# Kernel optimization log

Measured on AMD Instinct MI355X. Metric: run time of the kernel, lower is better.

## Reference

```python
import jax, jax.numpy as jnp
import numpy as np

N, F, K, D = 4096, 512, 8, 64


def setup_inputs() -> dict:
    key = jax.random.key(0)
    ks = jax.random.split(key, 6)
    H = jax.random.normal(ks[0], (N, F), dtype=jnp.float32)
    # dense 0/1 adjacency with self-loops
    A = jax.random.randint(ks[1], (N, N), 0, 2).astype(jnp.float32)
    A = jnp.maximum(A, jnp.eye(N, dtype=jnp.float32))
    idx = jnp.arange(N, dtype=jnp.int64)
    glorot_w = (2.0 / (F + D)) ** 0.5
    glorot_a = (2.0 / (D + 1)) ** 0.5
    kernels = glorot_w * jax.random.normal(ks[2], (K, F, D), dtype=jnp.float32)
    attn_kernels = glorot_a * jax.random.normal(ks[3], (K, 2, D, 1), dtype=jnp.float32)
    biases = 0.01 * jax.random.normal(ks[4], (K, D), dtype=jnp.float32)
    return {"H": H, "A": A, "idx": idx, "kernels": kernels,
            "attn_kernels": attn_kernels, "biases": biases}


def reference(H, A, idx, kernels, attn_kernels, biases):
    # (dropout is identity at inference)
    batch_A = A[:, idx]                                  # [N, N]
    HW = jnp.einsum('nf,kfd->knd', H, kernels)           # [K, N, D]
    a1 = attn_kernels[:, 0, :, 0]                        # [K, D]
    a2 = attn_kernels[:, 1, :, 0]                        # [K, D]
    s1 = jnp.einsum('knd,kd->kn', HW, a1)                # score_i (source)
    s2 = jnp.einsum('knd,kd->kn', HW, a2)                # score_j (target)
    scores = s1[:, :, None] + s2[:, None, :]             # [K, N, N]
    neg_big = jnp.finfo(jnp.float32).min
    scores = jnp.where(batch_A[None, :, :] == 0.0, neg_big, scores)
    # LeakyReLU(0.2) applied AFTER masking, as in the original
    scores = jnp.where(scores >= 0, scores, 0.2 * scores)
    attn = jax.nn.softmax(scores, axis=-1)               # [K, N, N]
    res = jnp.einsum('kij,kjd->kid', attn, HW) + biases[:, None, :]  # [K, N, D]
    out = jax.nn.elu(res)                                # is_last=False -> concat heads
    out = jnp.transpose(out, (1, 0, 2)).reshape(N, K * D)
    return out
```

## Files before the change

kernel.cpp:

```cpp
#include <hip/hip_runtime.h>
#include <hip/hip_fp16.h>
#include <float.h>
#include <math.h>

#define NN 4096
#define FF 512
#define KK 8
#define DD 64

typedef float f32x4 __attribute__((ext_vector_type(4)));
typedef _Float16 h2 __attribute__((ext_vector_type(2)));
typedef _Float16 f16x4 __attribute__((ext_vector_type(4)));
typedef _Float16 f16x8 __attribute__((ext_vector_type(8)));
typedef unsigned int u32;
typedef unsigned long long u64;

__device__ __forceinline__ h2 H2(u32 u) { union { u32 u; h2 h; } x; x.u = u; return x.h; }
__device__ __forceinline__ u32 U32(h2 h) { union { u32 u; h2 h; } x; x.h = h; return x.u; }
__device__ __forceinline__ u32 pmask(u32 m, int sh) {
  u32 b = (m >> sh) & 3u;
  return ((b * 0x10001u) & 0x20001u) * 0xFFFFu;
}

__global__ __launch_bounds__(256) void k_bits(const float* __restrict__ A,
                                              u64* __restrict__ bits) {
  const int gw = (blockIdx.x * 256 + threadIdx.x) >> 6;
  const int lane = threadIdx.x & 63;
  const int nw = (gridDim.x * 256) >> 6;
  const int totw = NN * NN / 64;
  for (int wd = gw; wd < totw; wd += nw) {
    float a = A[(size_t)wd * 64 + lane];
    u64 m = __ballot(a != 0.0f);
    if (lane == 0) bits[wd] = m;
  }
}

__global__ __launch_bounds__(256) void k_hf(const float* __restrict__ H,
                                            _Float16* __restrict__ HF) {
  const int w = threadIdx.x >> 6, lane = threadIdx.x & 63;
  const int tile = blockIdx.x * 4 + w;
  const int rb = tile >> 4, fb = tile & 15;
  const int l15 = lane & 15, grp = lane >> 4;
  const float* src = H + (size_t)(rb * 16 + l15) * FF + fb * 32 + grp * 4;
  float4 lo = *reinterpret_cast<const float4*>(src);
  float4 hi = *reinterpret_cast<const float4*>(src + 16);
  f16x8 v;
  v[0] = (_Float16)lo.x; v[1] = (_Float16)lo.y; v[2] = (_Float16)lo.z; v[3] = (_Float16)lo.w;
  v[4] = (_Float16)hi.x; v[5] = (_Float16)hi.y; v[6] = (_Float16)hi.z; v[7] = (_Float16)hi.w;
  *reinterpret_cast<f16x8*>(HF + (size_t)tile * 512 + lane * 8) = v;
}

__global__ __launch_bounds__(256) void k_wf(const float* __restrict__ Wk,
                                            _Float16* __restrict__ WF) {
  const int g = blockIdx.x * 256 + threadIdx.x;
  const int frag = g >> 6, lane = g & 63;
  const int k = frag >> 6, fb = (frag >> 2) & 15, db = frag & 3;
  const int l15 = lane & 15, grp = lane >> 4;
  f16x8 v;
  #pragma unroll
  for (int e = 0; e < 8; ++e) {
    int f = fb * 32 + grp * 4 + (e & 3) + 16 * (e >> 2);
    int d = db * 16 + l15;
    v[e] = (_Float16)Wk[((size_t)k * FF + f) * DD + d];
  }
  *reinterpret_cast<f16x8*>(WF + (size_t)frag * 512 + lane * 8) = v;
}

__global__ __launch_bounds__(256) void k_hw(const _Float16* __restrict__ HF,
                                            const _Float16* __restrict__ WF,
                                            const float* __restrict__ attk,
                                            _Float16* __restrict__ HWF,
                                            float* __restrict__ s1,
                                            float* __restrict__ s2) {
  __shared__ __align__(16) _Float16 Bs[64 * 512];
  const int w = threadIdx.x >> 6, lane = threadIdx.x & 63;
  const int k = blockIdx.y;
  const int rb = blockIdx.x * 4 + w;
  const int l15 = lane & 15, grp = lane >> 4;
  const _Float16* wfk = WF + (size_t)k * 64 * 512;
  #pragma unroll
  for (int c = 0; c < 16; ++c) {
    int chunk = c * 4 + w;
    *reinterpret_cast<f16x8*>(&Bs[chunk * 512 + lane * 8]) =
        *reinterpret_cast<const f16x8*>(wfk + (size_t)chunk * 512 + lane * 8);
  }
  __syncthreads();
  f32x4 acc[4] = {};
  for (int fb = 0; fb < 16; ++fb) {
    f16x8 a = *reinterpret_cast<const f16x8*>(HF + (size_t)(rb * 16 + fb) * 512 + lane * 8);
    #pragma unroll
    for (int n = 0; n < 4; ++n) {
      f16x8 b = *reinterpret_cast<const f16x8*>(&Bs[(fb * 4 + n) * 512 + lane * 8]);
      acc[n] = __builtin_amdgcn_mfma_f32_16x16x32_f16(a, b, acc[n], 0, 0, 0);
    }
  }
  const int jb = rb >> 1;
  const int half = rb & 1;
  #pragma unroll
  for (int db = 0; db < 4; ++db) {
    f16x4 v;
    #pragma unroll
    for (int q = 0; q < 4; ++q) v[q] = (_Float16)acc[db][q];
    *reinterpret_cast<f16x4*>(HWF + (size_t)((k * 128 + jb) * 4 + db) * 512 + lane * 8 + half * 4) = v;
  }
  float a1v[4], a2v[4];
  #pragma unroll
  for (int n = 0; n < 4; ++n) {
    a1v[n] = attk[k * 2 * DD + n * 16 + l15];
    a2v[n] = attk[k * 2 * DD + DD + n * 16 + l15];
  }
  #pragma unroll
  for (int q = 0; q < 4; ++q) {
    float p1 = 0.f, p2 = 0.f;
    #pragma unroll
    for (int n = 0; n < 4; ++n) { p1 += acc[n][q] * a1v[n]; p2 += acc[n][q] * a2v[n]; }
    #pragma unroll
    for (int off = 8; off; off >>= 1) { p1 += __shfl_xor(p1, off); p2 += __shfl_xor(p2, off); }
    if (l15 == 0) {
      int row = rb * 16 + grp * 4 + q;
      s1[k * NN + row] = p1;
      s2[k * NN + row] = p2;
    }
  }
}

__global__ __launch_bounds__(256) void k_mx(const float* __restrict__ s2,
                                            float* __restrict__ mx) {
  const int k = blockIdx.x, tid = threadIdx.x;
  float m = -FLT_MAX;
  for (int j = tid; j < NN; j += 256) m = fmaxf(m, s2[k * NN + j]);
  #pragma unroll
  for (int o = 32; o; o >>= 1) m = fmaxf(m, __shfl_xor(m, o));
  __shared__ float sm[4];
  if ((tid & 63) == 0) sm[tid >> 6] = m;
  __syncthreads();
  if (tid == 0) mx[k] = fmaxf(fmaxf(sm[0], sm[1]), fmaxf(sm[2], sm[3]));
}

__global__ __launch_bounds__(256, 2) void k_attn(
    const u64* __restrict__ bits, const _Float16* __restrict__ HWF,
    const float* __restrict__ s1, const float* __restrict__ s2,
    const float* __restrict__ mx,
    _Float16* __restrict__ pacc, float* __restrict__ pw) {
  __shared__ __align__(16) _Float16 epl[1024];
  __shared__ __align__(16) _Float16 enl[1024];
  const int k = blockIdx.y, jh = blockIdx.z;
  const int i0 = blockIdx.x * 256;
  const int tid = threadIdx.x;
  const int w = tid >> 6, lane = tid & 63, l15 = lane & 15, grp = lane >> 4;
  const int jbase = jh * 1024;
  const float mxk = mx[k];
  {
    float4 sv = *reinterpret_cast<const float4*>(&s2[k * NN + jbase + tid * 4]);
    f16x4 e4, n4;
    e4[0] = (_Float16)__expf(sv.x - mxk); e4[1] = (_Float16)__expf(sv.y - mxk);
    e4[2] = (_Float16)__expf(sv.z - mxk); e4[3] = (_Float16)__expf(sv.w - mxk);
    n4[0] = (_Float16)__expf(0.2f * (sv.x - mxk)); n4[1] = (_Float16)__expf(0.2f * (sv.y - mxk));
    n4[2] = (_Float16)__expf(0.2f * (sv.z - mxk)); n4[3] = (_Float16)__expf(0.2f * (sv.w - mxk));
    *reinterpret_cast<f16x4*>(&epl[tid * 4]) = e4;
    *reinterpret_cast<f16x4*>(&enl[tid * 4]) = n4;
  }
  __syncthreads();
  h2 P1h[4], Q1h[4];
  const u64* browp[4];
  #pragma unroll
  for (int s = 0; s < 4; ++s) {
    int row = i0 + w * 64 + s * 16 + l15;
    float s1r = s1[k * NN + row];
    float t = s1r + mxk;
    float cr = fmaxf(t, 0.2f * t);
    _Float16 p = (_Float16)__expf(t - cr);
    _Float16 q = (_Float16)__expf(0.2f * t - cr);
    P1h[s] = h2{p, p}; Q1h[s] = h2{q, q};
    browp[s] = bits + (size_t)row * (NN / 64) + (jbase >> 6);
  }
  const int g4 = grp * 4;
  const _Float16* hwb = HWF + ((size_t)(k * 128 + jh * 32) * 4) * 512 + lane * 8;
  const h2 ones = h2{(_Float16)1.0f, (_Float16)1.0f};
  f32x4 acc[4][4] = {};
  float wsum[4] = {};
  u64 bw[4];
  #pragma unroll
  for (int s = 0; s < 4; ++s) bw[s] = browp[s][0];
  for (int jw = 0; jw < 16; ++jw) {
    u64 nbw[4];
    const int nx = jw < 15 ? jw + 1 : 15;
    #pragma unroll
    for (int s = 0; s < 4; ++s) nbw[s] = browp[s][nx];
    #pragma unroll
    for (int js = 0; js < 2; ++js) {
      const int jl = jw * 64 + js * 32;
      f16x8 bf0 = *reinterpret_cast<const f16x8*>(hwb + ((jw * 2 + js) * 4 + 0) * 512);
      f16x8 bf1 = *reinterpret_cast<const f16x8*>(hwb + ((jw * 2 + js) * 4 + 1) * 512);
      f16x8 bf2 = *reinterpret_cast<const f16x8*>(hwb + ((jw * 2 + js) * 4 + 2) * 512);
      f16x8 bf3 = *reinterpret_cast<const f16x8*>(hwb + ((jw * 2 + js) * 4 + 3) * 512);
      f16x4 elo = *reinterpret_cast<const f16x4*>(&epl[jl + g4]);
      f16x4 ehi = *reinterpret_cast<const f16x4*>(&epl[jl + 16 + g4]);
      f16x4 nlo = *reinterpret_cast<const f16x4*>(&enl[jl + g4]);
      f16x4 nhi = *reinterpret_cast<const f16x4*>(&enl[jl + 16 + g4]);
      const u32 e01 = ((const u32*)&elo)[0], e23 = ((const u32*)&elo)[1];
      const u32 e45 = ((const u32*)&ehi)[0], e67 = ((const u32*)&ehi)[1];
      const u32 n01 = ((const u32*)&nlo)[0], n23 = ((const u32*)&nlo)[1];
      const u32 n45 = ((const u32*)&nhi)[0], n67 = ((const u32*)&nhi)[1];
      #pragma unroll
      for (int s = 0; s < 4; ++s) {
        const u32 m32 = (u32)(bw[s] >> (js * 32));
        u32 p0 = U32(__builtin_elementwise_max(P1h[s] * H2(e01), Q1h[s] * H2(n01))) & pmask(m32, g4);
        u32 p1 = U32(__builtin_elementwise_max(P1h[s] * H2(e23), Q1h[s] * H2(n23))) & pmask(m32, g4 + 2);
        u32 p2 = U32(__builtin_elementwise_max(P1h[s] * H2(e45), Q1h[s] * H2(n45))) & pmask(m32, g4 + 16);
        u32 p3 = U32(__builtin_elementwise_max(P1h[s] * H2(e67), Q1h[s] * H2(n67))) & pmask(m32, g4 + 18);
        wsum[s] = __builtin_amdgcn_fdot2(H2(p0), ones, wsum[s], false);
        wsum[s] = __builtin_amdgcn_fdot2(H2(p1), ones, wsum[s], false);
        wsum[s] = __builtin_amdgcn_fdot2(H2(p2), ones, wsum[s], false);
        wsum[s] = __builtin_amdgcn_fdot2(H2(p3), ones, wsum[s], false);
        union { u32 u[4]; f16x8 v; } af;
        af.u[0] = p0; af.u[1] = p1; af.u[2] = p2; af.u[3] = p3;
        acc[s][0] = __builtin_amdgcn_mfma_f32_16x16x32_f16(af.v, bf0, acc[s][0], 0, 0, 0);
        acc[s][1] = __builtin_amdgcn_mfma_f32_16x16x32_f16(af.v, bf1, acc[s][1], 0, 0, 0);
        acc[s][2] = __builtin_amdgcn_mfma_f32_16x16x32_f16(af.v, bf2, acc[s][2], 0, 0, 0);
        acc[s][3] = __builtin_amdgcn_mfma_f32_16x16x32_f16(af.v, bf3, acc[s][3], 0, 0, 0);
      }
    }
    #pragma unroll
    for (int s = 0; s < 4; ++s) bw[s] = nbw[s];
  }
  const size_t ob = (size_t)(jh * KK + k) * NN;
  #pragma unroll
  for (int s = 0; s < 4; ++s) {
    float ws = wsum[s];
    ws += __shfl_xor(ws, 16);
    ws += __shfl_xor(ws, 32);
    #pragma unroll
    for (int n = 0; n < 4; ++n)
      #pragma unroll
      for (int q = 0; q < 4; ++q) {
        int row = i0 + w * 64 + s * 16 + grp * 4 + q;
        pacc[(ob + row) * DD + n * 16 + l15] = (_Float16)acc[s][n][q];
      }
    if (grp == 0) {
      int row = i0 + w * 64 + s * 16 + l15;
      pw[ob + row] = ws;
    }
  }
}

__global__ __launch_bounds__(256) void k_merge(const _Float16* __restrict__ pacc,
                                               const float* __restrict__ pw,
                                               const float* __restrict__ bias,
                                               float* __restrict__ out) {
  const int o4 = blockIdx.x * 256 + threadIdx.x;
  const int i = o4 >> 7, rem = o4 & 127, k = rem >> 4, d4 = rem & 15;
  const size_t idx = ((size_t)k * NN + i) * DD + d4 * 4;
  float4 a = {0.f, 0.f, 0.f, 0.f};
  float wsum = 0.f;
  #pragma unroll
  for (int s = 0; s < 4; ++s) {
    f16x4 v = *reinterpret_cast<const f16x4*>(&pacc[(size_t)s * (KK * NN * DD) + idx]);
    a.x += (float)v[0]; a.y += (float)v[1]; a.z += (float)v[2]; a.w += (float)v[3];
    wsum += pw[(size_t)s * (KK * NN) + k * NN + i];
  }
  float rw = 1.0f / wsum;
  float4 bv = *reinterpret_cast<const float4*>(bias + k * DD + d4 * 4);
  float4 r;
  r.x = a.x * rw + bv.x; r.x = r.x > 0.f ? r.x : expm1f(r.x);
  r.y = a.y * rw + bv.y; r.y = r.y > 0.f ? r.y : expm1f(r.y);
  r.z = a.z * rw + bv.z; r.z = r.z > 0.f ? r.z : expm1f(r.z);
  r.w = a.w * rw + bv.w; r.w = r.w > 0.f ? r.w : expm1f(r.w);
  *reinterpret_cast<float4*>(out + (size_t)o4 * 4) = r;
}

extern "C" void kernel_launch(void* const* d_in, const int* in_sizes, int n_in,
                              void* d_out, int out_size, void* d_ws, size_t ws_size,
                              hipStream_t stream) {
  const float* H    = (const float*)d_in[0];
  const float* A    = (const float*)d_in[1];
  const float* Wk   = (const float*)d_in[3];
  const float* attk = (const float*)d_in[4];
  const float* bias = (const float*)d_in[5];
  float* out = (float*)d_out;

  char* base = (char*)d_ws;
  _Float16* HF  = (_Float16*)(base + 0);
  _Float16* WF  = (_Float16*)(base + 4194304);
  _Float16* HWF = (_Float16*)(base + 4718592);
  u64* bits     = (u64*)(base + 8912896);
  float* s1p    = (float*)(base + 11010048);
  float* s2p    = (float*)(base + 11141120);
  float* mxp    = (float*)(base + 11272192);
  _Float16* pacc = (_Float16*)(base + 11276288);
  float* pwp    = (float*)(base + 28053504);

  k_bits<<<2048, 256, 0, stream>>>(A, bits);
  k_hf<<<1024, 256, 0, stream>>>(H, HF);
  k_wf<<<128, 256, 0, stream>>>(Wk, WF);
  k_hw<<<dim3(NN / 64, KK), 256, 0, stream>>>(HF, WF, attk, HWF, s1p, s2p);
  k_mx<<<KK, 256, 0, stream>>>(s2p, mxp);
  k_attn<<<dim3(NN / 256, KK, 4), 256, 0, stream>>>(bits, HWF, s1p, s2p, mxp, pacc, pwp);
  k_merge<<<2048, 256, 0, stream>>>(pacc, pwp, bias, out);
}
```

Before: 176.2 us.

## Fuse merge into attention kernel, compute max via atomics, merge prep kernels

Merges the H and W fp16 conversion kernels into one launch. The per-head max is now taken inside the HW GEMM kernel with an order-preserving encoded atomicMax, so the separate max kernel goes away. The attention kernel changes to 512-thread blocks of 64 rows, with each wave covering a 512-column slice. Partial accumulators are reduced through LDS and the kernel writes normalised, bias-added, ELU'd output directly, removing the fp16 partial buffers and the merge kernel. This trades the global round-trip and extra launches for LDS reductions, more barriers, and a different occupancy and grid shape (512 blocks instead of 512 with 256 threads).

```diff
diff --git a/kernel.cpp b/kernel.cpp
--- a/kernel.cpp
+++ b/kernel.cpp
@@ -21,9 +21,19 @@
   u32 b = (m >> sh) & 3u;
   return ((b * 0x10001u) & 0x20001u) * 0xFFFFu;
 }
+__device__ __forceinline__ u32 encf(float f) {
+  u32 u = __float_as_uint(f);
+  return ((int)u < 0) ? ~u : (u | 0x80000000u);
+}
+__device__ __forceinline__ float decf(u32 e) {
+  u32 u = (e & 0x80000000u) ? (e ^ 0x80000000u) : ~e;
+  return __uint_as_float(u);
+}
 
 __global__ __launch_bounds__(256) void k_bits(const float* __restrict__ A,
-                                              u64* __restrict__ bits) {
+                                              u64* __restrict__ bits,
+                                              u32* __restrict__ mxu) {
+  if (blockIdx.x == 0 && threadIdx.x < KK) mxu[threadIdx.x] = 0u;
   const int gw = (blockIdx.x * 256 + threadIdx.x) >> 6;
   const int lane = threadIdx.x & 63;
   const int nw = (gridDim.x * 256) >> 6;
@@ -35,35 +45,36 @@
   }
 }
 
-__global__ __launch_bounds__(256) void k_hf(const float* __restrict__ H,
-                                            _Float16* __restrict__ HF) {
+__global__ __launch_bounds__(256) void k_prep(const float* __restrict__ H,
+                                              const float* __restrict__ Wk,
+                                              _Float16* __restrict__ HF,
+                                              _Float16* __restrict__ WF) {
   const int w = threadIdx.x >> 6, lane = threadIdx.x & 63;
-  const int tile = blockIdx.x * 4 + w;
-  const int rb = tile >> 4, fb = tile & 15;
   const int l15 = lane & 15, grp = lane >> 4;
-  const float* src = H + (size_t)(rb * 16 + l15) * FF + fb * 32 + grp * 4;
-  float4 lo = *reinterpret_cast<const float4*>(src);
-  float4 hi = *reinterpret_cast<const float4*>(src + 16);
-  f16x8 v;
-  v[0] = (_Float16)lo.x; v[1] = (_Float16)lo.y; v[2] = (_Float16)lo.z; v[3] = (_Float16)lo.w;
-  v[4] = (_Float16)hi.x; v[5] = (_Float16)hi.y; v[6] = (_Float16)hi.z; v[7] = (_Float16)hi.w;
-  *reinterpret_cast<f16x8*>(HF + (size_t)tile * 512 + lane * 8) = v;
-}
-
-__global__ __launch_bounds__(256) void k_wf(const float* __restrict__ Wk,
-                                            _Float16* __restrict__ WF) {
-  const int g = blockIdx.x * 256 + threadIdx.x;
-  const int frag = g >> 6, lane = g & 63;
-  const int k = frag >> 6, fb = (frag >> 2) & 15, db = frag & 3;
-  const int l15 = lane & 15, grp = lane >> 4;
-  f16x8 v;
-  #pragma unroll
-  for (int e = 0; e < 8; ++e) {
-    int f = fb * 32 + grp * 4 + (e & 3) + 16 * (e >> 2);
-    int d = db * 16 + l15;
-    v[e] = (_Float16)Wk[((size_t)k * FF + f) * DD + d];
-  }
-  *reinterpret_cast<f16x8*>(WF + (size_t)frag * 512 + lane * 8) = v;
+  if (blockIdx.x < 1024) {
+    const int tile = blockIdx.x * 4 + w;
+    const int rb = tile >> 4, fb = tile & 15;
+    const float* src = H + (size_t)(rb * 16 + l15) * FF + fb * 32 + grp * 4;
+    float4 lo = *reinterpret_cast<const float4*>(src);
+    float4 hi = *reinterpret_cast<const float4*>(src + 16);
+    f16x8 v;
+    v[0] = (_Float16)lo.x; v[1] = (_Float16)lo.y; v[2] = (_Float16)lo.z; v[3] = (_Float16)lo.w;
+    v[4] = (_Float16)hi.x; v[5] = (_Float16)hi.y; v[6] = (_Float16)hi.z; v[7] = (_Float16)hi.w;
+    *reinterpret_cast<f16x8*>(HF + (size_t)tile * 512 + lane * 8) = v;
+  } else {
+    const int g = (blockIdx.x - 1024) * 256 + threadIdx.x;
+    const int frag = g >> 6, fl = g & 63;
+    const int fl15 = fl & 15, fgrp = fl >> 4;
+    const int k = frag >> 6, fb = (frag >> 2) & 15, db = frag & 3;
+    f16x8 v;
+    #pragma unroll
+    for (int e = 0; e < 8; ++e) {
+      int f = fb * 32 + fgrp * 4 + (e & 3) + 16 * (e >> 2);
+      int d = db * 16 + fl15;
+      v[e] = (_Float16)Wk[((size_t)k * FF + f) * DD + d];
+    }
+    *reinterpret_cast<f16x8*>(WF + (size_t)frag * 512 + fl * 8) = v;
+  }
 }
 
 __global__ __launch_bounds__(256) void k_hw(const _Float16* __restrict__ HF,
@@ -71,8 +82,10 @@
                                             const float* __restrict__ attk,
                                             _Float16* __restrict__ HWF,
                                             float* __restrict__ s1,
-                                            float* __restrict__ s2) {
+                                            float* __restrict__ s2,
+                                            u32* __restrict__ mxu) {
   __shared__ __align__(16) _Float16 Bs[64 * 512];
+  __shared__ float wmax[4];
   const int w = threadIdx.x >> 6, lane = threadIdx.x & 63;
   const int k = blockIdx.y;
   const int rb = blockIdx.x * 4 + w;
@@ -86,13 +99,17 @@
   }
   __syncthreads();
   f32x4 acc[4] = {};
+  f16x8 a_cur = *reinterpret_cast<const f16x8*>(HF + (size_t)(rb * 16) * 512 + lane * 8);
   for (int fb = 0; fb < 16; ++fb) {
-    f16x8 a = *reinterpret_cast<const f16x8*>(HF + (size_t)(rb * 16 + fb) * 512 + lane * 8);
+    f16x8 a_nxt = a_cur;
+    if (fb < 15)
+      a_nxt = *reinterpret_cast<const f16x8*>(HF + (size_t)(rb * 16 + fb + 1) * 512 + lane * 8);
     #pragma unroll
     for (int n = 0; n < 4; ++n) {
       f16x8 b = *reinterpret_cast<const f16x8*>(&Bs[(fb * 4 + n) * 512 + lane * 8]);
-      acc[n] = __builtin_amdgcn_mfma_f32_16x16x32_f16(a, b, acc[n], 0, 0, 0);
-    }
+      acc[n] = __builtin_amdgcn_mfma_f32_16x16x32_f16(a_cur, b, acc[n], 0, 0, 0);
+    }
+    a_cur = a_nxt;
   }
   const int jb = rb >> 1;
   const int half = rb & 1;
@@ -109,6 +126,7 @@
     a1v[n] = attk[k * 2 * DD + n * 16 + l15];
     a2v[n] = attk[k * 2 * DD + DD + n * 16 + l15];
   }
+  float pm2 = -FLT_MAX;
   #pragma unroll
   for (int q = 0; q < 4; ++q) {
     float p1 = 0.f, p2 = 0.f;
@@ -121,79 +139,88 @@
       s1[k * NN + row] = p1;
       s2[k * NN + row] = p2;
     }
-  }
-}
-
-__global__ __launch_bounds__(256) void k_mx(const float* __restrict__ s2,
-                                            float* __restrict__ mx) {
-  const int k = blockIdx.x, tid = threadIdx.x;
-  float m = -FLT_MAX;
-  for (int j = tid; j < NN; j += 256) m = fmaxf(m, s2[k * NN + j]);
-  #pragma unroll
-  for (int o = 32; o; o >>= 1) m = fmaxf(m, __shfl_xor(m, o));
-  __shared__ float sm[4];
-  if ((tid & 63) == 0) sm[tid >> 6] = m;
-  __syncthreads();
-  if (tid == 0) mx[k] = fmaxf(fmaxf(sm[0], sm[1]), fmaxf(sm[2], sm[3]));
-}
-
-__global__ __launch_bounds__(256, 2) void k_attn(
+    pm2 = fmaxf(pm2, p2);
+  }
+  pm2 = fmaxf(pm2, __shfl_xor(pm2, 16));
+  pm2 = fmaxf(pm2, __shfl_xor(pm2, 32));
+  if (lane == 0) wmax[w] = pm2;
+  __syncthreads();
+  if (threadIdx.x == 0) {
+    float bm = fmaxf(fmaxf(wmax[0], wmax[1]), fmaxf(wmax[2], wmax[3]));
+    atomicMax(&mxu[k], encf(bm));
+  }
+}
+
+__global__ __launch_bounds__(512, 4) void k_attn(
     const u64* __restrict__ bits, const _Float16* __restrict__ HWF,
     const float* __restrict__ s1, const float* __restrict__ s2,
-    const float* __restrict__ mx,
-    _Float16* __restrict__ pacc, float* __restrict__ pw) {
-  __shared__ __align__(16) _Float16 epl[1024];
-  __shared__ __align__(16) _Float16 enl[1024];
-  const int k = blockIdx.y, jh = blockIdx.z;
-  const int i0 = blockIdx.x * 256;
+    const u32* __restrict__ mxu, const float* __restrict__ bias,
+    float* __restrict__ out) {
+  __shared__ __align__(16) _Float16 epl[4096];
+  __shared__ __align__(16) _Float16 enl[4096];
+  __shared__ _Float16 surf[4][64][68];
+  __shared__ float wsumLDS[8][64];
+  __shared__ float rtot[64];
+  const int k = blockIdx.y;
+  const int i0 = blockIdx.x * 64;
   const int tid = threadIdx.x;
   const int w = tid >> 6, lane = tid & 63, l15 = lane & 15, grp = lane >> 4;
-  const int jbase = jh * 1024;
-  const float mxk = mx[k];
+  const float mxk = decf(mxu[k]);
   {
-    float4 sv = *reinterpret_cast<const float4*>(&s2[k * NN + jbase + tid * 4]);
-    f16x4 e4, n4;
-    e4[0] = (_Float16)__expf(sv.x - mxk); e4[1] = (_Float16)__expf(sv.y - mxk);
-    e4[2] = (_Float16)__expf(sv.z - mxk); e4[3] = (_Float16)__expf(sv.w - mxk);
-    n4[0] = (_Float16)__expf(0.2f * (sv.x - mxk)); n4[1] = (_Float16)__expf(0.2f * (sv.y - mxk));
-    n4[2] = (_Float16)__expf(0.2f * (sv.z - mxk)); n4[3] = (_Float16)__expf(0.2f * (sv.w - mxk));
-    *reinterpret_cast<f16x4*>(&epl[tid * 4]) = e4;
-    *reinterpret_cast<f16x4*>(&enl[tid * 4]) = n4;
-  }
-  __syncthreads();
+    float4 sa = *reinterpret_cast<const float4*>(&s2[k * NN + tid * 8]);
+    float4 sb = *reinterpret_cast<const float4*>(&s2[k * NN + tid * 8 + 4]);
+    f16x4 e0, e1, n0, n1;
+    e0[0] = (_Float16)__expf(sa.x - mxk); e0[1] = (_Float16)__expf(sa.y - mxk);
+    e0[2] = (_Float16)__expf(sa.z - mxk); e0[3] = (_Float16)__expf(sa.w - mxk);
+    e1[0] = (_Float16)__expf(sb.x - mxk); e1[1] = (_Float16)__expf(sb.y - mxk);
+    e1[2] = (_Float16)__expf(sb.z - mxk); e1[3] = (_Float16)__expf(sb.w - mxk);
+    n0[0] = (_Float16)__expf(0.2f * (sa.x - mxk)); n0[1] = (_Float16)__expf(0.2f * (sa.y - mxk));
+    n0[2] = (_Float16)__expf(0.2f * (sa.z - mxk)); n0[3] = (_Float16)__expf(0.2f * (sa.w - mxk));
+    n1[0] = (_Float16)__expf(0.2f * (sb.x - mxk)); n1[1] = (_Float16)__expf(0.2f * (sb.y - mxk));
+    n1[2] = (_Float16)__expf(0.2f * (sb.z - mxk)); n1[3] = (_Float16)__expf(0.2f * (sb.w - mxk));
+    *reinterpret_cast<f16x4*>(&epl[tid * 8])     = e0;
+    *reinterpret_cast<f16x4*>(&epl[tid * 8 + 4]) = e1;
+    *reinterpret_cast<f16x4*>(&enl[tid * 8])     = n0;
+    *reinterpret_cast<f16x4*>(&enl[tid * 8 + 4]) = n1;
+  }
   h2 P1h[4], Q1h[4];
-  const u64* browp[4];
+  const u64* brp[4];
   #pragma unroll
   for (int s = 0; s < 4; ++s) {
-    int row = i0 + w * 64 + s * 16 + l15;
+    int row = i0 + s * 16 + l15;
     float s1r = s1[k * NN + row];
     float t = s1r + mxk;
     float cr = fmaxf(t, 0.2f * t);
     _Float16 p = (_Float16)__expf(t - cr);
     _Float16 q = (_Float16)__expf(0.2f * t - cr);
     P1h[s] = h2{p, p}; Q1h[s] = h2{q, q};
-    browp[s] = bits + (size_t)row * (NN / 64) + (jbase >> 6);
-  }
+    brp[s] = bits + (size_t)row * (NN / 64) + w * 8;
+  }
+  float biasv[4];
+  #pragma unroll
+  for (int n = 0; n < 4; ++n) biasv[n] = bias[k * DD + n * 16 + l15];
+  __syncthreads();
   const int g4 = grp * 4;
-  const _Float16* hwb = HWF + ((size_t)(k * 128 + jh * 32) * 4) * 512 + lane * 8;
+  const _Float16* hwb = HWF + ((size_t)(k * 128 + w * 16) * 4) * 512 + lane * 8;
   const h2 ones = h2{(_Float16)1.0f, (_Float16)1.0f};
   f32x4 acc[4][4] = {};
   float wsum[4] = {};
   u64 bw[4];
   #pragma unroll
-  for (int s = 0; s < 4; ++s) bw[s] = browp[s][0];
-  for (int jw = 0; jw < 16; ++jw) {
+  for (int s = 0; s < 4; ++s) bw[s] = brp[s][0];
+  for (int jw = 0; jw < 8; ++jw) {
     u64 nbw[4];
-    const int nx = jw < 15 ? jw + 1 : 15;
-    #pragma unroll
-    for (int s = 0; s < 4; ++s) nbw[s] = browp[s][nx];
-    #pragma unroll
-    for (int js = 0; js < 2; ++js) {
-      const int jl = jw * 64 + js * 32;
-      f16x8 bf0 = *reinterpret_cast<const f16x8*>(hwb + ((jw * 2 + js) * 4 + 0) * 512);
-      f16x8 bf1 = *reinterpret_cast<const f16x8*>(hwb + ((jw * 2 + js) * 4 + 1) * 512);
-      f16x8 bf2 = *reinterpret_cast<const f16x8*>(hwb + ((jw * 2 + js) * 4 + 2) * 512);
-      f16x8 bf3 = *reinterpret_cast<const f16x8*>(hwb + ((jw * 2 + js) * 4 + 3) * 512);
+    const int nx = jw < 7 ? jw + 1 : 7;
+    #pragma unroll
+    for (int s = 0; s < 4; ++s) nbw[s] = brp[s][nx];
+    #pragma unroll
+    for (int hf = 0; hf < 2; ++hf) {
+      const int js = jw * 2 + hf;
+      const int jl = w * 512 + js * 32;
+      f16x8 bf0 = *reinterpret_cast<const f16x8*>(hwb + (js * 4 + 0) * 512);
+      f16x8 bf1 = *reinterpret_cast<const f16x8*>(hwb + (js * 4 + 1) * 512);
+      f16x8 bf2 = *reinterpret_cast<const f16x8*>(hwb + (js * 4 + 2) * 512);
+      f16x8 bf3 = *reinterpret_cast<const f16x8*>(hwb + (js * 4 + 3) * 512);
       f16x4 elo = *reinterpret_cast<const f16x4*>(&epl[jl + g4]);
       f16x4 ehi = *reinterpret_cast<const f16x4*>(&epl[jl + 16 + g4]);
       f16x4 nlo = *reinterpret_cast<const f16x4*>(&enl[jl + g4]);
@@ -204,7 +231,7 @@
       const u32 n45 = ((const u32*)&nhi)[0], n67 = ((const u32*)&nhi)[1];
       #pragma unroll
       for (int s = 0; s < 4; ++s) {
-        const u32 m32 = (u32)(bw[s] >> (js * 32));
+        const u32 m32 = (u32)(bw[s] >> (hf * 32));
         u32 p0 = U32(__builtin_elementwise_max(P1h[s] * H2(e01), Q1h[s] * H2(n01))) & pmask(m32, g4);
         u32 p1 = U32(__builtin_elementwise_max(P1h[s] * H2(e23), Q1h[s] * H2(n23))) & pmask(m32, g4 + 2);
         u32 p2 = U32(__builtin_elementwise_max(P1h[s] * H2(e45), Q1h[s] * H2(n45))) & pmask(m32, g4 + 16);
@@ -224,49 +251,67 @@
     #pragma unroll
     for (int s = 0; s < 4; ++s) bw[s] = nbw[s];
   }
-  const size_t ob = (size_t)(jh * KK + k) * NN;
   #pragma unroll
   for (int s = 0; s < 4; ++s) {
-    float ws = wsum[s];
-    ws += __shfl_xor(ws, 16);
-    ws += __shfl_xor(ws, 32);
-    #pragma unroll
-    for (int n = 0; n < 4; ++n)
+    wsum[s] += __shfl_xor(wsum[s], 16);
+    wsum[s] += __shfl_xor(wsum[s], 32);
+  }
+  auto store_surf = [&](int id) {
+    #pragma unroll
+    for (int s = 0; s < 4; ++s)
+      #pragma unroll
+      for (int n = 0; n < 4; ++n)
+        #pragma unroll
+        for (int q = 0; q < 4; ++q)
+          surf[id][s * 16 + grp * 4 + q][n * 16 + l15] = (_Float16)acc[s][n][q];
+  };
+  auto add_surf = [&](int id) {
+    #pragma unroll
+    for (int s = 0; s < 4; ++s)
+      #pragma unroll
+      for (int n = 0; n < 4; ++n)
+        #pragma unroll
+        for (int q = 0; q < 4; ++q)
+          acc[s][n][q] += (float)surf[id][s * 16 + grp * 4 + q][n * 16 + l15];
+  };
+  if (w >= 4) store_surf(w - 4);
+  if (grp == 0) {
+    #pragma unroll
+    for (int s = 0; s < 4; ++s) wsumLDS[w][s * 16 + l15] = wsum[s];
+  }
+  __syncthreads();
+  if (w < 4) add_surf(w);
+  if (tid < 64) {
+    float t = 0.f;
+    #pragma unroll
+    for (int w8 = 0; w8 < 8; ++w8) t += wsumLDS[w8][tid];
+    rtot[tid] = 1.0f / t;
+  }
+  if (w == 2 || w == 3) store_surf(w);
+  __syncthreads();
+  if (w < 2) add_surf(w + 2);
+  if (w == 0) store_surf(0);
+  if (w == 1) store_surf(1);
+  __syncthreads();
+  if (w == 0) add_surf(1);
+  if (w == 1) add_surf(0);
+  if (w < 2) {
+    #pragma unroll
+    for (int si = 0; si < 2; ++si) {
+      const int s = w * 2 + si;
       #pragma unroll
       for (int q = 0; q < 4; ++q) {
-        int row = i0 + w * 64 + s * 16 + grp * 4 + q;
-        pacc[(ob + row) * DD + n * 16 + l15] = (_Float16)acc[s][n][q];
+        const int row = s * 16 + grp * 4 + q;
+        const float rw = rtot[row];
+        #pragma unroll
+        for (int n = 0; n < 4; ++n) {
+          float v = acc[s][n][q] * rw + biasv[n];
+          v = v > 0.f ? v : expm1f(v);
+          out[(size_t)(i0 + row) * (KK * DD) + k * DD + n * 16 + l15] = v;
+        }
       }
-    if (grp == 0) {
-      int row = i0 + w * 64 + s * 16 + l15;
-      pw[ob + row] = ws;
-    }
-  }
-}
-
-__global__ __launch_bounds__(256) void k_merge(const _Float16* __restrict__ pacc,
-                                               const float* __restrict__ pw,
-                                               const float* __restrict__ bias,
-                                               float* __restrict__ out) {
-  const int o4 = blockIdx.x * 256 + threadIdx.x;
-  const int i = o4 >> 7, rem = o4 & 127, k = rem >> 4, d4 = rem & 15;
-  const size_t idx = ((size_t)k * NN + i) * DD + d4 * 4;
-  float4 a = {0.f, 0.f, 0.f, 0.f};
-  float wsum = 0.f;
-  #pragma unroll
-  for (int s = 0; s < 4; ++s) {
-    f16x4 v = *reinterpret_cast<const f16x4*>(&pacc[(size_t)s * (KK * NN * DD) + idx]);
-    a.x += (float)v[0]; a.y += (float)v[1]; a.z += (float)v[2]; a.w += (float)v[3];
-    wsum += pw[(size_t)s * (KK * NN) + k * NN + i];
-  }
-  float rw = 1.0f / wsum;
-  float4 bv = *reinterpret_cast<const float4*>(bias + k * DD + d4 * 4);
-  float4 r;
-  r.x = a.x * rw + bv.x; r.x = r.x > 0.f ? r.x : expm1f(r.x);
-  r.y = a.y * rw + bv.y; r.y = r.y > 0.f ? r.y : expm1f(r.y);
-  r.z = a.z * rw + bv.z; r.z = r.z > 0.f ? r.z : expm1f(r.z);
-  r.w = a.w * rw + bv.w; r.w = r.w > 0.f ? r.w : expm1f(r.w);
-  *reinterpret_cast<float4*>(out + (size_t)o4 * 4) = r;
+    }
+  }
 }
 
 extern "C" void kernel_launch(void* const* d_in, const int* in_sizes, int n_in,
@@ -286,15 +331,10 @@
   u64* bits     = (u64*)(base + 8912896);
   float* s1p    = (float*)(base + 11010048);
   float* s2p    = (float*)(base + 11141120);
-  float* mxp    = (float*)(base + 11272192);
-  _Float16* pacc = (_Float16*)(base + 11276288);
-  float* pwp    = (float*)(base + 28053504);
-
-  k_bits<<<2048, 256, 0, stream>>>(A, bits);
-  k_hf<<<1024, 256, 0, stream>>>(H, HF);
-  k_wf<<<128, 256, 0, stream>>>(Wk, WF);
-  k_hw<<<dim3(NN / 64, KK), 256, 0, stream>>>(HF, WF, attk, HWF, s1p, s2p);
-  k_mx<<<KK, 256, 0, stream>>>(s2p, mxp);
-  k_attn<<<dim3(NN / 256, KK, 4), 256, 0, stream>>>(bits, HWF, s1p, s2p, mxp, pacc, pwp);
-  k_merge<<<2048, 256, 0, stream>>>(pacc, pwp, bias, out);
-}
+  u32* mxu      = (u32*)(base + 11272192);
+
+  k_bits<<<2048, 256, 0, stream>>>(A, bits, mxu);
+  k_prep<<<1152, 256, 0, stream>>>(H, Wk, HF, WF);
+  k_hw<<<dim3(NN / 64, KK), 256, 0, stream>>>(HF, WF, attk, HWF, s1p, s2p, mxu);
+  k_attn<<<dim3(NN / 64, KK), 512, 0, stream>>>(bits, HWF, s1p, s2p, mxu, bias, out);
+}
```

After: 285.3 us. 1.62x slower.
